# Optimization experiments

Hardware: AMD Instinct MI355X
Metric: run time of the kernel (lower is better)

Reference implementation:

```python
import jax, jax.numpy as jnp
import numpy as np
from jax import lax

B, T, D, H = 4, 4096, 1024, 8
DK, DV = 1024, 2048          # expand_k=1.0, expand_v=2.0
RANK, MAXL, LOOPD = 16, 8, 128  # lora_rank, max_loops, dim*loop_dim_fraction
THRESH = 0.99
EPS = 1e-6
GK_SCALE = 16.0              # GLA forget-gate temperature


def setup_inputs() -> dict:
    key = jax.random.key(0)
    ks = jax.random.split(key, 16)
    r = lambda i, shape, s=0.02: jax.random.normal(ks[i], shape, jnp.float32) * s
    return {
        "h": jax.random.normal(ks[0], (B, T, D), jnp.float32),
        "e": jax.random.normal(ks[1], (B, T, D), jnp.float32),
        "norm_w": jnp.ones((D,), jnp.float32),
        "out_norm_w": jnp.ones((D,), jnp.float32),
        "Wq": r(2, (D, DK)), "Wk": r(3, (D, DK)), "Wv": r(4, (D, DV)),
        "Wgk": r(5, (D, DK)), "Wg": r(6, (D, DV)), "Wo": r(7, (DV, D)),
        "lora_A": r(8, (MAXL, D, RANK)), "lora_B": r(9, (MAXL, RANK, D)),
        "inj_A": 0.9 * jnp.eye(D, dtype=jnp.float32) + r(10, (D, D)),
        "inj_B": r(11, (D, D)),
        "act_w": r(12, (D,)),
        "act_b": jnp.full((), -2.0, jnp.float32),  # gradual halting
        "loop_table": r(13, (MAXL, LOOPD)),
        "n_loops": 4,
    }


def rmsnorm(x, w):
    return x * lax.rsqrt(jnp.mean(x * x, axis=-1, keepdims=True) + EPS) * w


def gla(x, Wq, Wk, Wv, Wgk, Wg, Wo, num_heads):
    """Gated Linear Attention: data-dependent forget gates, linear-time recurrent scan."""
    b, t, d = x.shape
    dk, dv = Wq.shape[1], Wv.shape[1]
    dkh, dvh = dk // num_heads, dv // num_heads
    q = (x @ Wq).reshape(b, t, num_heads, dkh) * (dkh ** -0.5)
    k = (x @ Wk).reshape(b, t, num_heads, dkh)
    v = (x @ Wv).reshape(b, t, num_heads, dvh)
    # forget gate alpha in (0,1): exp(logsigmoid(gk)/16)
    alpha = jnp.exp(jax.nn.log_sigmoid(x @ Wgk) / GK_SCALE).reshape(b, t, num_heads, dkh)

    def step(S, qkva):  # S: (b, H, dkh, dvh)
        qt, kt, vt, at = qkva
        S = at[..., None] * S + kt[..., None] * vt[..., None, :]
        ot = jnp.einsum('bhk,bhkv->bhv', qt, S)
        return S, ot

    S0 = jnp.zeros((b, num_heads, dkh, dvh), x.dtype)
    xs = (jnp.swapaxes(q, 0, 1), jnp.swapaxes(k, 0, 1),
          jnp.swapaxes(v, 0, 1), jnp.swapaxes(alpha, 0, 1))
    _, o = lax.scan(step, S0, xs)                  # o: (t, b, H, dvh)
    o = jnp.swapaxes(o, 0, 1).reshape(b, t, dv)
    o = o * jax.nn.silu(x @ Wg)                    # output gate
    return o @ Wo


def reference(h, e, norm_w, out_norm_w, Wq, Wk, Wv, Wgk, Wg, Wo,
              lora_A, lora_B, inj_A, inj_B, act_w, act_b, loop_table, n_loops):
    b, t_len, d = h.shape
    halted = jnp.zeros((b, t_len), bool)
    cum = jnp.zeros((b, t_len), h.dtype)
    h_out = jnp.zeros_like(h)
    loopd = loop_table.shape[1]
    for t in range(n_loops):  # small fixed depth loop (structurally distinct LoRA/embed per t)
        # loop index embedding on first loopd channels
        h = h.at[..., :loopd].add(loop_table[t])
        h_norm = rmsnorm(h + e, norm_w)
        g = gla(h_norm, Wq, Wk, Wv, Wgk, Wg, Wo, H)   # dropout: eval mode (identity)
        g = g + (g @ lora_A[t]) @ lora_B[t]            # depth LoRA
        h = h @ inj_A.T + e @ inj_B.T + g              # LTI injection: A.h + B.e + gla
        # ACT halting accumulate
        p = jax.nn.sigmoid(h @ act_w + act_b)          # (b, t_len)
        running = ~halted
        p_eff = jnp.where(running, p, jnp.zeros_like(p))
        new_cum = cum + p_eff
        newly = running & (new_cum >= THRESH)
        w = jnp.where(newly, 1.0 - cum, p_eff)         # remainder for newly-halted
        h_out = h_out + w[..., None] * h
        cum = new_cum
        halted = halted | newly
    return rmsnorm(h_out, out_norm_w)
```

## Files before the change

### kernel.cpp

```cpp
#include <hip/hip_runtime.h>

#define BB 4
#define TT 4096
#define DD 1024
#define HH 8
#define DKK 1024
#define DVV 2048
#define MR (BB*TT)
#define DKH 128
#define DVH 256
#define NLOOPS 4
#define LCH 128
#define NCH (TT/LCH)
#define PADW 136
#define NPROJ 7168

#define WS_NEED 662310912ull

__device__ __attribute__((aligned(256))) unsigned char g_ws[WS_NEED];

typedef __bf16 bf16x8 __attribute__((ext_vector_type(8)));
typedef float  f32x4  __attribute__((ext_vector_type(4)));

union GemmSmem {
    unsigned short ab[2][128 * 32];
    unsigned short c16[128 * 136];
    float cf[64 * 140];
};

__device__ __forceinline__ unsigned short f2bfu(float f) {
    unsigned int u = __builtin_bit_cast(unsigned int, f);
    u += 0x7fffu + ((u >> 16) & 1u);
    return (unsigned short)(u >> 16);
}
__device__ __forceinline__ float bfu2f(unsigned short s) {
    unsigned int u = ((unsigned int)s) << 16;
    return __builtin_bit_cast(float, u);
}

__device__ __forceinline__ void gld_lds16(const void* g, void* l) {
    __builtin_amdgcn_global_load_lds(
        (__attribute__((address_space(1))) void*)const_cast<void*>(g),
        (__attribute__((address_space(3))) void*)l, 16, 0, 0);
}

__global__ __launch_bounds__(256) void k_transpose_bf16(
    const float* __restrict__ in, unsigned short* __restrict__ out, int K, int N)
{
    __shared__ float tile[64][65];
    int k0 = blockIdx.y * 64, n0 = blockIdx.x * 64;
    int tx = threadIdx.x & 63, ty = threadIdx.x >> 6;
    #pragma unroll
    for (int r = 0; r < 64; r += 4)
        tile[ty + r][tx] = in[(size_t)(k0 + ty + r) * N + n0 + tx];
    __syncthreads();
    #pragma unroll
    for (int r = 0; r < 64; r += 4)
        out[(size_t)(n0 + ty + r) * K + k0 + tx] = f2bfu(tile[tx][ty + r]);
}

__global__ __launch_bounds__(256) void k_conv_e(
    const float* __restrict__ e, unsigned short* __restrict__ he)
{
    size_t gid = (size_t)blockIdx.x * 256 + threadIdx.x;
    size_t b4 = gid * 4;
    size_t row = b4 >> 10; int col = (int)(b4 & 1023);
    float4 v = *(const float4*)&e[row * 1024 + col];
    *(ushort4*)&he[row * 2048 + 1024 + col] =
        make_ushort4(f2bfu(v.x), f2bfu(v.y), f2bfu(v.z), f2bfu(v.w));
}

__global__ __launch_bounds__(256) void k_conv_injcomb(
    const float* __restrict__ injA, const float* __restrict__ injB,
    unsigned short* __restrict__ WinjT, float* __restrict__ diag)
{
    int idx = blockIdx.x * 256 + threadIdx.x;
    int i = idx >> 10, j = idx & 1023;
    float va = injA[idx], vb = injB[idx];
    unsigned short ua;
    if (i == j) { diag[i] = va; ua = 0; }
    else        { ua = f2bfu(va); }
    WinjT[(size_t)i * 2048 + j] = ua;
    WinjT[(size_t)i * 2048 + 1024 + j] = f2bfu(vb);
}

__global__ __launch_bounds__(256) void k_prep(
    float* __restrict__ h, const float* __restrict__ e,
    const float* __restrict__ norm_w, const float* __restrict__ ltab,
    unsigned short* __restrict__ he, unsigned short* __restrict__ xn_bf)
{
    int row = blockIdx.x, tid = threadIdx.x;
    size_t base = (size_t)row * DD + tid * 4;
    float4 hv = *(float4*)&h[base];
    if (tid < 32) {
        float4 lv = *(const float4*)&ltab[tid * 4];
        hv.x += lv.x; hv.y += lv.y; hv.z += lv.z; hv.w += lv.w;
        *(float4*)&h[base] = hv;
    }
    float4 ev = *(const float4*)&e[base];
    float sx = hv.x + ev.x, sy = hv.y + ev.y, sz = hv.z + ev.z, sw = hv.w + ev.w;
    float partial = sx*sx + sy*sy + sz*sz + sw*sw;
    __shared__ float red[256];
    red[tid] = partial; __syncthreads();
    for (int st = 128; st > 0; st >>= 1) {
        if (tid < st) red[tid] += red[tid + st];
        __syncthreads();
    }
    float rms = rsqrtf(red[0] * (1.0f / DD) + 1e-6f);
    float4 wv = *(const float4*)&norm_w[tid * 4];
    *(ushort4*)&xn_bf[base] = make_ushort4(
        f2bfu(sx * rms * wv.x), f2bfu(sy * rms * wv.y),
        f2bfu(sz * rms * wv.z), f2bfu(sw * rms * wv.w));
    *(ushort4*)&he[(size_t)row * 2048 + tid * 4] =
        make_ushort4(f2bfu(hv.x), f2bfu(hv.y), f2bfu(hv.z), f2bfu(hv.w));
}

__global__ __launch_bounds__(256) void k_gemm_proj(
    const unsigned short* __restrict__ A, const unsigned short* __restrict__ Bt,
    unsigned short* __restrict__ qout, unsigned short* __restrict__ kout,
    float* __restrict__ lgout, unsigned short* __restrict__ vout,
    unsigned short* __restrict__ xgout, float qscale)
{
    __shared__ GemmSmem sm;
    unsigned short* lsA = sm.ab[0];
    unsigned short* lsB = sm.ab[1];
    int tid = threadIdx.x, lane = tid & 63, wave = tid >> 6;
    int wm = wave >> 1, wn = wave & 1;
    int bm = blockIdx.y * 128, bn = blockIdx.x * 128;
    int lrow = lane >> 2, lcol = (lane & 3) * 8;
    const int K = 1024;

    f32x4 acc[4][4];
    #pragma unroll
    for (int i = 0; i < 4; ++i)
        #pragma unroll
        for (int j = 0; j < 4; ++j) { f32x4 z = {0,0,0,0}; acc[i][j] = z; }

    for (int k0 = 0; k0 < K; k0 += 32) {
        __syncthreads();
        #pragma unroll
        for (int r = 0; r < 2; ++r) {
            int row = r * 64 + wave * 16 + lrow;
            gld_lds16(A  + (size_t)(bm + row) * K + k0 + lcol, &lsA[row * 32 + lcol]);
            gld_lds16(Bt + (size_t)(bn + row) * K + k0 + lcol, &lsB[row * 32 + lcol]);
        }
        __syncthreads();
        int quad = lane >> 4, mr = lane & 15;
        bf16x8 av[4], bv[4];
        #pragma unroll
        for (int t2 = 0; t2 < 4; ++t2) {
            av[t2] = *(const bf16x8*)&lsA[(wm * 64 + t2 * 16 + mr) * 32 + quad * 8];
            bv[t2] = *(const bf16x8*)&lsB[(wn * 64 + t2 * 16 + mr) * 32 + quad * 8];
        }
        #pragma unroll
        for (int tm = 0; tm < 4; ++tm)
            #pragma unroll
            for (int tn = 0; tn < 4; ++tn)
                acc[tm][tn] = __builtin_amdgcn_mfma_f32_16x16x32_bf16(
                    av[tm], bv[tn], acc[tm][tn], 0, 0, 0);
    }

    int quad = lane >> 4, mr = lane & 15;
    __syncthreads();

    if (bn >= 2048 && bn < 3072) {
        int cb = bn - 2048;
        #pragma unroll 1
        for (int half = 0; half < 2; ++half) {
            if (wm == half) {
                #pragma unroll
                for (int tm = 0; tm < 4; ++tm)
                    #pragma unroll
                    for (int tn = 0; tn < 4; ++tn)
                        #pragma unroll
                        for (int r = 0; r < 4; ++r) {
                            float v = acc[tm][tn][r];
                            v = (fminf(v, 0.f) - log1pf(expf(-fabsf(v)))) * 0.0625f;
                            sm.cf[(tm * 16 + quad * 4 + r) * 140 + wn * 64 + tn * 16 + mr] = v;
                        }
            }
            __syncthreads();
            #pragma unroll
            for (int ps = 0; ps < 8; ++ps) {
                int idx = ps * 256 + tid;
                int rl = idx >> 5, c4 = (idx & 31) * 4;
                float4 vv = *(float4*)&sm.cf[rl * 140 + c4];
                *(float4*)&lgout[(size_t)(bm + half * 64 + rl) * 1024 + cb + c4] = vv;
            }
            __syncthreads();
        }
    } else {
        unsigned short* obuf; int stride, cb;
        float scale = 1.f;
        if (bn < 1024)      { obuf = qout;  stride = 1024; cb = bn;        scale = qscale; }
        else if (bn < 2048) { obuf = kout;  stride = 1024; cb = bn - 1024; }
        else if (bn < 5120) { obuf = vout;  stride = 2048; cb = bn - 3072; }
        else                { obuf = xgout; stride = 2048; cb = bn - 5120; }
        #pragma unroll
        for (int tm = 0; tm < 4; ++tm)
            #pragma unroll
            for (int tn = 0; tn < 4; ++tn)
                #pragma unroll
                for (int r = 0; r < 4; ++r)
                    sm.c16[(wm * 64 + tm * 16 + quad * 4 + r) * 136
                           + wn * 64 + tn * 16 + mr] = f2bfu(acc[tm][tn][r] * scale);
        __syncthreads();
        #pragma unroll
        for (int ps = 0; ps < 8; ++ps) {
            int idx = ps * 256 + tid;
            int rl = idx >> 4, c8 = (idx & 15) * 8;
            int4 w = *(int4*)&sm.c16[rl * 136 + c8];
            *(int4*)&obuf[(size_t)(bm + rl) * stride + cb + c8] = w;
        }
    }
}

template<int HASADD, int HASDIAG>
__global__ __launch_bounds__(256) void k_gemm_f32(
    const unsigned short* __restrict__ A, const unsigned short* __restrict__ Bt,
    float* __restrict__ out, const float* __restrict__ addend,
    const float* __restrict__ hsrc, const float* __restrict__ diag,
    int N, int K)
{
    __shared__ GemmSmem sm;
    unsigned short* lsA = sm.ab[0];
    unsigned short* lsB = sm.ab[1];
    int tid = threadIdx.x, lane = tid & 63, wave = tid >> 6;
    int wm = wave >> 1, wn = wave & 1;
    int bm = blockIdx.y * 128, bn = blockIdx.x * 128;
    int lrow = lane >> 2, lcol = (lane & 3) * 8;

    f32x4 acc[4][4];
    #pragma unroll
    for (int i = 0; i < 4; ++i)
        #pragma unroll
        for (int j = 0; j < 4; ++j) { f32x4 z = {0,0,0,0}; acc[i][j] = z; }

    for (int k0 = 0; k0 < K; k0 += 32) {
        __syncthreads();
        #pragma unroll
        for (int r = 0; r < 2; ++r) {
            int row = r * 64 + wave * 16 + lrow;
            gld_lds16(A  + (size_t)(bm + row) * K + k0 + lcol, &lsA[row * 32 + lcol]);
            gld_lds16(Bt + (size_t)(bn + row) * K + k0 + lcol, &lsB[row * 32 + lcol]);
        }
        __syncthreads();
        int quad = lane >> 4, mr = lane & 15;
        bf16x8 av[4], bv[4];
        #pragma unroll
        for (int t2 = 0; t2 < 4; ++t2) {
            av[t2] = *(const bf16x8*)&lsA[(wm * 64 + t2 * 16 + mr) * 32 + quad * 8];
            bv[t2] = *(const bf16x8*)&lsB[(wn * 64 + t2 * 16 + mr) * 32 + quad * 8];
        }
        #pragma unroll
        for (int tm = 0; tm < 4; ++tm)
            #pragma unroll
            for (int tn = 0; tn < 4; ++tn)
                acc[tm][tn] = __builtin_amdgcn_mfma_f32_16x16x32_bf16(
                    av[tm], bv[tn], acc[tm][tn], 0, 0, 0);
    }

    int quad = lane >> 4, mr = lane & 15;
    __syncthreads();
    #pragma unroll 1
    for (int half = 0; half < 2; ++half) {
        if (wm == half) {
            #pragma unroll
            for (int tm = 0; tm < 4; ++tm)
                #pragma unroll
                for (int tn = 0; tn < 4; ++tn)
                    #pragma unroll
                    for (int r = 0; r < 4; ++r)
                        sm.cf[(tm * 16 + quad * 4 + r) * 140
                              + wn * 64 + tn * 16 + mr] = acc[tm][tn][r];
        }
        __syncthreads();
        #pragma unroll
        for (int ps = 0; ps < 8; ++ps) {
            int idx = ps * 256 + tid;
            int rl = idx >> 5, c4 = (idx & 31) * 4;
            float4 vv = *(float4*)&sm.cf[rl * 140 + c4];
            size_t oi = (size_t)(bm + half * 64 + rl) * N + bn + c4;
            if (HASDIAG) {
                float4 hh = *(const float4*)&hsrc[oi];
                float4 dd = *(const float4*)&diag[bn + c4];
                vv.x += hh.x * dd.x; vv.y += hh.y * dd.y;
                vv.z += hh.z * dd.z; vv.w += hh.w * dd.w;
            }
            if (HASADD) {
                float4 aa = *(const float4*)&addend[oi];
                vv.x += aa.x; vv.y += aa.y; vv.z += aa.z; vv.w += aa.w;
            }
            *(float4*)&out[oi] = vv;
        }
        __syncthreads();
    }
}

__global__ __launch_bounds__(128) void k_c1(
    const float* __restrict__ lg, unsigned short* __restrict__ q,
    unsigned short* __restrict__ kk, float* __restrict__ dLe)
{
    int chunk = blockIdx.x, bh = blockIdx.y;
    int b = bh >> 3, h = bh & 7;
    int i = threadIdx.x;
    size_t r0 = (size_t)b * TT + (size_t)chunk * LCH;
    float c = 0.f, e = 1.f;
    for (int t = 0; t < LCH; ++t) {
        size_t off = (r0 + t) * DKK + h * DKH + i;
        c += lg[off];
        e = __expf(c);
        float ei = __expf(-c);
        q[off] = f2bfu(bfu2f(q[off]) * e);
        kk[off] = f2bfu(bfu2f(kk[off]) * ei);
    }
    dLe[((size_t)chunk * 32 + bh) * DKH + i] = e;
}

__global__ __launch_bounds__(256, 1) void k_c2(
    const unsigned short* __restrict__ q, const unsigned short* __restrict__ kk,
    const unsigned short* __restrict__ v, unsigned short* __restrict__ ob,
    float* __restrict__ U)
{
    extern __shared__ unsigned short smd[];
    unsigned short* lQ  = smd;
    unsigned short* lK  = smd + LCH * PADW;
    unsigned short* lKT = smd + 2 * LCH * PADW;
    unsigned short* lVT = smd + 3 * LCH * PADW;

    int chunk = blockIdx.x, bh = blockIdx.y;
    int b = bh >> 3, h = bh & 7;
    int tid = threadIdx.x, lane = tid & 63, wave = tid >> 6;
    int wm = wave >> 1, wn = wave & 1;
    int quad = lane >> 4, mr = lane & 15;
    size_t r0 = (size_t)b * TT + (size_t)chunk * LCH;

    #pragma unroll
    for (int ps = 0; ps < 8; ++ps) {
        int idx = ps * 256 + tid;
        int row = idx >> 4, c8 = (idx & 15) * 8;
        size_t g = (r0 + row) * DKK + h * DKH + c8;
        *(int4*)&lQ[row * PADW + c8] = *(const int4*)&q[g];
        union { int4 w; unsigned short u[8]; } tmp;
        tmp.w = *(const int4*)&kk[g];
        *(int4*)&lK[row * PADW + c8] = tmp.w;
        #pragma unroll
        for (int u2 = 0; u2 < 8; ++u2)
            lKT[(c8 + u2) * PADW + row] = tmp.u[u2];
    }
    __syncthreads();

    f32x4 pa[4][4];
    #pragma unroll
    for (int i = 0; i < 4; ++i)
        #pragma unroll
        for (int j = 0; j < 4; ++j) { f32x4 z = {0,0,0,0}; pa[i][j] = z; }
    for (int k0 = 0; k0 < DKH; k0 += 32) {
        bf16x8 av[4], bv[4];
        #pragma unroll
        for (int t2 = 0; t2 < 4; ++t2) {
            av[t2] = *(const bf16x8*)&lQ[(wm * 64 + t2 * 16 + mr) * PADW + k0 + quad * 8];
            bv[t2] = *(const bf16x8*)&lK[(wn * 64 + t2 * 16 + mr) * PADW + k0 + quad * 8];
        }
        #pragma unroll
        for (int tm = 0; tm < 4; ++tm)
            #pragma unroll
            for (int tn = 0; tn < 4; ++tn)
                pa[tm][tn] = __builtin_amdgcn_mfma_f32_16x16x32_bf16(
                    av[tm], bv[tn], pa[tm][tn], 0, 0, 0);
    }
    __syncthreads();

    #pragma unroll
    for (int tm = 0; tm < 4; ++tm)
        #pragma unroll
        for (int tn = 0; tn < 4; ++tn)
            #pragma unroll
            for (int r = 0; r < 4; ++r) {
                int trow = wm * 64 + tm * 16 + quad * 4 + r;
                int scol = wn * 64 + tn * 16 + mr;
                float pv = (trow >= scol) ? pa[tm][tn][r] : 0.f;
                lQ[trow * PADW + scol] = f2bfu(pv);
            }
    #pragma unroll
    for (int ps = 0; ps < 8; ++ps) {
        int idx = ps * 256 + tid;
        int s = idx >> 4, j8 = (idx & 15) * 8;
        size_t g = (r0 + s) * DVV + h * DVH + j8;
        union { int4 w; unsigned short u[8]; } tmp;
        tmp.w = *(const int4*)&v[g];
        #pragma unroll
        for (int u2 = 0; u2 < 8; ++u2)
            lVT[(j8 + u2) * PADW + s] = tmp.u[u2];
    }
    __syncthreads();

    #pragma unroll 1
    for (int panel = 0; panel < 2; ++panel) {
        f32x4 oa[4][4], ua[4][4];
        #pragma unroll
        for (int i = 0; i < 4; ++i)
            #pragma unroll
            for (int j = 0; j < 4; ++j) { f32x4 z = {0,0,0,0}; oa[i][j] = z; ua[i][j] = z; }
        for (int k0 = 0; k0 < LCH; k0 += 32) {
            bf16x8 pv[4], kt[4], vb[4];
            #pragma unroll
            for (int t2 = 0; t2 < 4; ++t2) {
                pv[t2] = *(const bf16x8*)&lQ [(wm * 64 + t2 * 16 + mr) * PADW + k0 + quad * 8];
                kt[t2] = *(const bf16x8*)&lKT[(wm * 64 + t2 * 16 + mr) * PADW + k0 + quad * 8];
                vb[t2] = *(const bf16x8*)&lVT[(wn * 64 + t2 * 16 + mr) * PADW + k0 + quad * 8];
            }
            #pragma unroll
            for (int tm = 0; tm < 4; ++tm)
                #pragma unroll
                for (int tn = 0; tn < 4; ++tn) {
                    oa[tm][tn] = __builtin_amdgcn_mfma_f32_16x16x32_bf16(
                        pv[tm], vb[tn], oa[tm][tn], 0, 0, 0);
                    ua[tm][tn] = __builtin_amdgcn_mfma_f32_16x16x32_bf16(
                        kt[tm], vb[tn], ua[tm][tn], 0, 0, 0);
                }
        }
        #pragma unroll
        for (int tm = 0; tm < 4; ++tm)
            #pragma unroll
            for (int tn = 0; tn < 4; ++tn)
                #pragma unroll
                for (int r = 0; r < 4; ++r) {
                    int m_ = wm * 64 + tm * 16 + quad * 4 + r;
                    int j_ = panel * 128 + wn * 64 + tn * 16 + mr;
                    ob[(r0 + m_) * DVV + h * DVH + j_] = f2bfu(oa[tm][tn][r]);
                    U[(((size_t)chunk * 32 + bh) * DKH + m_) * DVH + j_] = ua[tm][tn][r];
                }
        __syncthreads();
        if (panel == 0) {
            #pragma unroll
            for (int ps = 0; ps < 8; ++ps) {
                int idx = ps * 256 + tid;
                int s = idx >> 4, j8 = (idx & 15) * 8;
                size_t g = (r0 + s) * DVV + h * DVH + 128 + j8;
                union { int4 w; unsigned short u[8]; } tmp;
                tmp.w = *(const int4*)&v[g];
                #pragma unroll
                for (int u2 = 0; u2 < 8; ++u2)
                    lVT[(j8 + u2) * PADW + s] = tmp.u[u2];
            }
            __syncthreads();
        }
    }
}

__global__ __launch_bounds__(256) void k_c3(
    float* __restrict__ U, const float* __restrict__ dLe)
{
    int gid = blockIdx.x * 256 + threadIdx.x;
    int bh = gid >> 13;
    int rem = gid & 8191;
    int i = rem >> 6, j4 = rem & 63;
    float4 S = make_float4(0.f, 0.f, 0.f, 0.f);
    for (int c = 0; c < NCH; ++c) {
        size_t off = (((size_t)c * 32 + bh) * DKH + i) * DVH + j4 * 4;
        float4 u = *(float4*)&U[off];
        *(float4*)&U[off] = S;
        float d = dLe[((size_t)c * 32 + bh) * DKH + i];
        S.x = d * (S.x + u.x); S.y = d * (S.y + u.y);
        S.z = d * (S.z + u.z); S.w = d * (S.w + u.w);
    }
}

__global__ __launch_bounds__(256, 1) void k_c4(
    const unsigned short* __restrict__ q, const float* __restrict__ S,
    unsigned short* __restrict__ ob, const unsigned short* __restrict__ xg)
{
    extern __shared__ unsigned short smd[];
    unsigned short* lQ  = smd;
    unsigned short* lST = smd + LCH * PADW;

    int chunk = blockIdx.x, bh = blockIdx.y;
    int b = bh >> 3, h = bh & 7;
    int tid = threadIdx.x, lane = tid & 63, wave = tid >> 6;
    int wm = wave >> 1, wn = wave & 1;
    int quad = lane >> 4, mr = lane & 15;
    size_t r0 = (size_t)b * TT + (size_t)chunk * LCH;

    #pragma unroll
    for (int ps = 0; ps < 8; ++ps) {
        int idx = ps * 256 + tid;
        int row = idx >> 4, c8 = (idx & 15) * 8;
        size_t g = (r0 + row) * DKK + h * DKH + c8;
        *(int4*)&lQ[row * PADW + c8] = *(const int4*)&q[g];
    }

    #pragma unroll 1
    for (int panel = 0; panel < 2; ++panel) {
        __syncthreads();
        #pragma unroll
        for (int ps = 0; ps < 16; ++ps) {
            int idx = ps * 256 + tid;
            int i = idx >> 5, j4 = idx & 31;
            float4 sv = *(const float4*)&S[(((size_t)chunk * 32 + bh) * DKH + i) * DVH
                                           + panel * 128 + j4 * 4];
            lST[(j4 * 4 + 0) * PADW + i] = f2bfu(sv.x);
            lST[(j4 * 4 + 1) * PADW + i] = f2bfu(sv.y);
            lST[(j4 * 4 + 2) * PADW + i] = f2bfu(sv.z);
            lST[(j4 * 4 + 3) * PADW + i] = f2bfu(sv.w);
        }
        __syncthreads();

        f32x4 oa[4][4];
        #pragma unroll
        for (int i = 0; i < 4; ++i)
            #pragma unroll
            for (int j = 0; j < 4; ++j) { f32x4 z = {0,0,0,0}; oa[i][j] = z; }
        for (int k0 = 0; k0 < DKH; k0 += 32) {
            bf16x8 av[4], bv[4];
            #pragma unroll
            for (int t2 = 0; t2 < 4; ++t2) {
                av[t2] = *(const bf16x8*)&lQ [(wm * 64 + t2 * 16 + mr) * PADW + k0 + quad * 8];
                bv[t2] = *(const bf16x8*)&lST[(wn * 64 + t2 * 16 + mr) * PADW + k0 + quad * 8];
            }
            #pragma unroll
            for (int tm = 0; tm < 4; ++tm)
                #pragma unroll
                for (int tn = 0; tn < 4; ++tn)
                    oa[tm][tn] = __builtin_amdgcn_mfma_f32_16x16x32_bf16(
                        av[tm], bv[tn], oa[tm][tn], 0, 0, 0);
        }
        #pragma unroll
        for (int tm = 0; tm < 4; ++tm)
            #pragma unroll
            for (int tn = 0; tn < 4; ++tn)
                #pragma unroll
                for (int r = 0; r < 4; ++r) {
                    int t_ = wm * 64 + tm * 16 + quad * 4 + r;
                    int j_ = panel * 128 + wn * 64 + tn * 16 + mr;
                    size_t oi = (r0 + t_) * DVV + h * DVH + j_;
                    float ov = bfu2f(ob[oi]) + oa[tm][tn][r];
                    float xf = bfu2f(xg[oi]);
                    ob[oi] = f2bfu(ov * xf / (1.f + expf(-xf)));
                }
    }
}

__global__ __launch_bounds__(256) void k_lora1(
    const float* __restrict__ G, const float* __restrict__ A, float* __restrict__ tmp)
{
    int row = blockIdx.x * 4 + (threadIdx.x >> 6);
    int lane = threadIdx.x & 63;
    float acc[16];
    #pragma unroll
    for (int r = 0; r < 16; ++r) acc[r] = 0.f;
    const float* grow = G + (size_t)row * DD;
    for (int k2 = lane; k2 < DD; k2 += 64) {
        float g = grow[k2];
        const float4* ar = (const float4*)(A + k2 * 16);
        float4 a0 = ar[0], a1 = ar[1], a2 = ar[2], a3 = ar[3];
        acc[0] = fmaf(g, a0.x, acc[0]);  acc[1] = fmaf(g, a0.y, acc[1]);
        acc[2] = fmaf(g, a0.z, acc[2]);  acc[3] = fmaf(g, a0.w, acc[3]);
        acc[4] = fmaf(g, a1.x, acc[4]);  acc[5] = fmaf(g, a1.y, acc[5]);
        acc[6] = fmaf(g, a1.z, acc[6]);  acc[7] = fmaf(g, a1.w, acc[7]);
        acc[8] = fmaf(g, a2.x, acc[8]);  acc[9] = fmaf(g, a2.y, acc[9]);
        acc[10] = fmaf(g, a2.z, acc[10]); acc[11] = fmaf(g, a2.w, acc[11]);
        acc[12] = fmaf(g, a3.x, acc[12]); acc[13] = fmaf(g, a3.y, acc[13]);
        acc[14] = fmaf(g, a3.z, acc[14]); acc[15] = fmaf(g, a3.w, acc[15]);
    }
    #pragma unroll
    for (int off = 32; off >= 1; off >>= 1)
        #pragma unroll
        for (int r = 0; r < 16; ++r) acc[r] += __shfl_xor(acc[r], off);
    if (lane == 0) {
        #pragma unroll
        for (int r = 0; r < 16; ++r) tmp[(size_t)row * 16 + r] = acc[r];
    }
}

__global__ __launch_bounds__(256) void k_lora2(
    float* __restrict__ G, const float* __restrict__ tmp, const float* __restrict__ Bm)
{
    int row = blockIdx.x, tid = threadIdx.x;
    __shared__ float t16[16];
    if (tid < 16) t16[tid] = tmp[(size_t)row * 16 + tid];
    __syncthreads();
    size_t base = (size_t)row * DD + tid * 4;
    float4 acc = *(float4*)&G[base];
    #pragma unroll
    for (int r = 0; r < 16; ++r) {
        float tv = t16[r];
        float4 bv = *(const float4*)&Bm[r * DD + tid * 4];
        acc.x = fmaf(tv, bv.x, acc.x); acc.y = fmaf(tv, bv.y, acc.y);
        acc.z = fmaf(tv, bv.z, acc.z); acc.w = fmaf(tv, bv.w, acc.w);
    }
    *(float4*)&G[base] = acc;
}

__global__ __launch_bounds__(256) void k_act(
    const float* __restrict__ h, const float* __restrict__ act_w,
    const float* __restrict__ act_b, float* __restrict__ out,
    float* __restrict__ cum, int* __restrict__ halted)
{
    int row = blockIdx.x, tid = threadIdx.x;
    size_t base = (size_t)row * DD + tid * 4;
    float4 hv = *(const float4*)&h[base];
    float4 wv = *(const float4*)&act_w[tid * 4];
    float partial = hv.x*wv.x + hv.y*wv.y + hv.z*wv.z + hv.w*wv.w;
    __shared__ float red[256];
    __shared__ float s_cm;
    __shared__ int s_hl;
    if (tid == 0) { s_cm = cum[row]; s_hl = halted[row]; }
    red[tid] = partial; __syncthreads();
    for (int st = 128; st > 0; st >>= 1) {
        if (tid < st) red[tid] += red[tid + st];
        __syncthreads();
    }
    float p = 1.f / (1.f + expf(-(red[0] + act_b[0])));
    float cm = s_cm;
    int hl = s_hl;
    float p_eff = hl ? 0.f : p;
    float ncum = cm + p_eff;
    int newly = (!hl) && (ncum >= 0.99f);
    float w = newly ? (1.f - cm) : p_eff;
    float4 ho = *(float4*)&out[base];
    ho.x += w * hv.x; ho.y += w * hv.y; ho.z += w * hv.z; ho.w += w * hv.w;
    *(float4*)&out[base] = ho;
    if (tid == 0) { cum[row] = ncum; halted[row] = hl | newly; }
}

__global__ __launch_bounds__(256) void k_final(
    float* __restrict__ io, const float* __restrict__ w)
{
    int row = blockIdx.x, tid = threadIdx.x;
    size_t base = (size_t)row * DD + tid * 4;
    float4 hv = *(const float4*)&io[base];
    float partial = hv.x*hv.x + hv.y*hv.y + hv.z*hv.z + hv.w*hv.w;
    __shared__ float red[256];
    red[tid] = partial; __syncthreads();
    for (int st = 128; st > 0; st >>= 1) {
        if (tid < st) red[tid] += red[tid + st];
        __syncthreads();
    }
    float rms = rsqrtf(red[0] * (1.0f / DD) + 1e-6f);
    float4 wv = *(const float4*)&w[tid * 4];
    float4 o = make_float4(hv.x*rms*wv.x, hv.y*rms*wv.y, hv.z*rms*wv.z, hv.w*rms*wv.w);
    *(float4*)&io[base] = o;
}

extern "C" void kernel_launch(void* const* d_in, const int* in_sizes, int n_in,
                              void* d_out, int out_size, void* d_ws, size_t ws_size,
                              hipStream_t stream)
{
    const float* in_h       = (const float*)d_in[0];
    const float* in_e       = (const float*)d_in[1];
    const float* norm_w     = (const float*)d_in[2];
    const float* out_norm_w = (const float*)d_in[3];
    const float* Wq   = (const float*)d_in[4];
    const float* Wk   = (const float*)d_in[5];
    const float* Wv   = (const float*)d_in[6];
    const float* Wgk  = (const float*)d_in[7];
    const float* Wg   = (const float*)d_in[8];
    const float* Wo   = (const float*)d_in[9];
    const float* lora_A = (const float*)d_in[10];
    const float* lora_B = (const float*)d_in[11];
    const float* inj_A  = (const float*)d_in[12];
    const float* inj_B  = (const float*)d_in[13];
    const float* act_w  = (const float*)d_in[14];
    const float* act_b  = (const float*)d_in[15];
    const float* loop_table = (const float*)d_in[16];

    char* p;
    if (ws_size >= WS_NEED) {
        p = (char*)d_ws;
    } else {
        void* sym = nullptr;
        hipGetSymbolAddress(&sym, HIP_SYMBOL(g_ws));
        p = (char*)sym;
    }

    float* h      = (float*)p;            p += (size_t)MR * DD * 4;
    unsigned short* he_bf = (unsigned short*)p; p += (size_t)MR * 2048 * 2;
    unsigned short* xn_bf = (unsigned short*)p; p += (size_t)MR * DD * 2;
    unsigned short* q_bf  = (unsigned short*)p; p += (size_t)MR * DKK * 2;
    unsigned short* k_bf  = (unsigned short*)p; p += (size_t)MR * DKK * 2;
    unsigned short* v_bf  = (unsigned short*)p; p += (size_t)MR * DVV * 2;
    unsigned short* xg_bf = (unsigned short*)p; p += (size_t)MR * DVV * 2;
    float* lgbuf  = (float*)p;            p += (size_t)MR * DKK * 4;
    unsigned short* ob0   = (unsigned short*)p; p += (size_t)MR * DVV * 2;
    float* U      = (float*)p;            p += (size_t)NCH * 32 * DKH * DVH * 4;
    float* dLe    = (float*)p;            p += (size_t)NCH * 32 * DKH * 4;
    unsigned short* WprojT = (unsigned short*)p; p += (size_t)NPROJ * DKK * 2;
    unsigned short* WoT    = (unsigned short*)p; p += (size_t)DD * DVV * 2;
    unsigned short* WinjT  = (unsigned short*)p; p += (size_t)DD * 2048 * 2;
    float* diagA = (float*)p;             p += DD * 4;
    float* tmp16 = (float*)p;             p += (size_t)MR * 16 * 4;
    float* cum   = (float*)p;             p += MR * 4;
    int*   halted = (int*)p;              p += MR * 4;
    float* g2 = lgbuf;
    float* h_out = (float*)d_out;

    hipMemcpyAsync(h, in_h, (size_t)MR * DD * 4, hipMemcpyDeviceToDevice, stream);
    hipMemsetAsync(h_out, 0, (size_t)MR * DD * 4, stream);
    hipMemsetAsync(cum, 0, MR * 4, stream);
    hipMemsetAsync(halted, 0, MR * 4, stream);

    k_transpose_bf16<<<dim3(16, 16), 256, 0, stream>>>(Wq,  WprojT,              DD, DKK);
    k_transpose_bf16<<<dim3(16, 16), 256, 0, stream>>>(Wk,  WprojT + 1024*1024,  DD, DKK);
    k_transpose_bf16<<<dim3(16, 16), 256, 0, stream>>>(Wgk, WprojT + 2048*1024,  DD, DKK);
    k_transpose_bf16<<<dim3(32, 16), 256, 0, stream>>>(Wv,  WprojT + 3072*1024,  DD, DVV);
    k_transpose_bf16<<<dim3(32, 16), 256, 0, stream>>>(Wg,  WprojT + (size_t)5120*1024, DD, DVV);
    k_transpose_bf16<<<dim3(16, 32), 256, 0, stream>>>(Wo,  WoT, DVV, DD);
    k_conv_injcomb<<<4096, 256, 0, stream>>>(inj_A, inj_B, WinjT, diagA);
    k_conv_e<<<MR * DD / 1024, 256, 0, stream>>>(in_e, he_bf);

    const float qscale = 0.08838834764831845f;

    for (int t = 0; t < NLOOPS; ++t) {
        k_prep<<<MR, 256, 0, stream>>>(h, in_e, norm_w, loop_table + t * 128, he_bf, xn_bf);

        k_gemm_proj<<<dim3(NPROJ/128, MR/128), 256, 0, stream>>>(
            xn_bf, WprojT, q_bf, k_bf, lgbuf, v_bf, xg_bf, qscale);

        k_c1<<<dim3(NCH, 32), 128, 0, stream>>>(lgbuf, q_bf, k_bf, dLe);
        k_c2<<<dim3(NCH, 32), 256, 4 * LCH * PADW * 2, stream>>>(
            q_bf, k_bf, v_bf, ob0, U);
        k_c3<<<1024, 256, 0, stream>>>(U, dLe);
        k_c4<<<dim3(NCH, 32), 256, 2 * LCH * PADW * 2, stream>>>(q_bf, U, ob0, xg_bf);

        k_gemm_f32<0,0><<<dim3(DD/128, MR/128), 256, 0, stream>>>(
            ob0, WoT, g2, nullptr, nullptr, nullptr, DD, DVV);

        k_lora1<<<MR / 4, 256, 0, stream>>>(g2, lora_A + (size_t)t * DD * 16, tmp16);
        k_lora2<<<MR, 256, 0, stream>>>(g2, tmp16, lora_B + (size_t)t * 16 * DD);

        k_gemm_f32<1,1><<<dim3(DD/128, MR/128), 256, 0, stream>>>(
            he_bf, WinjT, h, g2, h, diagA, DD, 2048);

        k_act<<<MR, 256, 0, stream>>>(h, act_w, act_b, h_out, cum, halted);
    }

    k_final<<<MR, 256, 0, stream>>>(h_out, out_norm_w);
}
```

Before: 4.818 ms.

## Replace GEMMs with 256x256 8-wave double-buffered swizzled LDS kernels

Measured after the change: 4.257 ms. 11.7% less time.

```diff
diff --git a/kernel.cpp b/kernel.cpp
--- a/kernel.cpp
+++ b/kernel.cpp
@@ -22,12 +22,6 @@
 typedef __bf16 bf16x8 __attribute__((ext_vector_type(8)));
 typedef float  f32x4  __attribute__((ext_vector_type(4)));
 
-union GemmSmem {
-    unsigned short ab[2][128 * 32];
-    unsigned short c16[128 * 136];
-    float cf[64 * 140];
-};
-
 __device__ __forceinline__ unsigned short f2bfu(float f) {
     unsigned int u = __builtin_bit_cast(unsigned int, f);
     u += 0x7fffu + ((u >> 16) & 1u);
@@ -115,79 +109,139 @@
         make_ushort4(f2bfu(hv.x), f2bfu(hv.y), f2bfu(hv.z), f2bfu(hv.w));
 }
 
-__global__ __launch_bounds__(256) void k_gemm_proj(
+template<int KB>
+__device__ __forceinline__ void gemm8_core(
+    const char* __restrict__ Ab, const char* __restrict__ Bb,
+    int bm, int bn, char* sm, f32x4 (&acc)[8][4])
+{
+    constexpr int NKT = KB / 128;
+    const int tid = threadIdx.x;
+    const int lane = tid & 63;
+    const int wave = tid >> 6;
+    const int wm = wave >> 2, wn = wave & 3;
+    const int ln15 = lane & 15, q4 = lane >> 4;
+    const int xorv = (ln15 & 7) << 4;
+    const int xc0 = (q4 * 16) ^ xorv;
+    const int xc1 = (64 + q4 * 16) ^ xorv;
+
+    const int L0 = tid * 16;
+    const int L1 = 8192 + tid * 16;
+    const int lin0 = L0 ^ (((L0 >> 7) & 7) << 4);
+    const int lin1 = L1 ^ (((L1 >> 7) & 7) << 4);
+    const int sr0 = lin0 >> 7, sc0 = lin0 & 127;
+    const int sr1 = lin1 >> 7, sc1 = lin1 & 127;
+
+    auto STAGE = [&](const char* gb, int row0, int kcol, int region) {
+        gld_lds16(gb + (size_t)(row0 + sr0) * KB + (kcol + sc0), sm + region + L0);
+        gld_lds16(gb + (size_t)(row0 + sr1) * KB + (kcol + sc1), sm + region + L1);
+    };
+    auto STAGE_R = [&](int r, int bufo, int kcol) {
+        if (r == 0)      STAGE(Ab, bm,       kcol, bufo);
+        else if (r == 1) STAGE(Bb, bn,       kcol, bufo + 32768);
+        else if (r == 2) STAGE(Bb, bn + 128, kcol, bufo + 49152);
+        else             STAGE(Ab, bm + 128, kcol, bufo + 16384);
+    };
+    auto QUAD = [&](int r, int bufo) {
+        const int mh = r >> 1, nh = r & 1;
+        const char* As = sm + bufo;
+        const char* Bs = sm + bufo + 32768;
+        bf16x8 av[4][2], bv[2][2];
+        #pragma unroll
+        for (int i2 = 0; i2 < 4; ++i2) {
+            const char* rp = As + (mh * 128 + wm * 64 + i2 * 16 + ln15) * 128;
+            av[i2][0] = *(const bf16x8*)(rp + xc0);
+            av[i2][1] = *(const bf16x8*)(rp + xc1);
+        }
+        #pragma unroll
+        for (int j2 = 0; j2 < 2; ++j2) {
+            const char* rp = Bs + (nh * 128 + wn * 32 + j2 * 16 + ln15) * 128;
+            bv[j2][0] = *(const bf16x8*)(rp + xc0);
+            bv[j2][1] = *(const bf16x8*)(rp + xc1);
+        }
+        __builtin_amdgcn_s_setprio(1);
+        #pragma unroll
+        for (int i2 = 0; i2 < 4; ++i2)
+            #pragma unroll
+            for (int j2 = 0; j2 < 2; ++j2) {
+                acc[mh*4+i2][nh*2+j2] = __builtin_amdgcn_mfma_f32_16x16x32_bf16(
+                    av[i2][0], bv[j2][0], acc[mh*4+i2][nh*2+j2], 0, 0, 0);
+                acc[mh*4+i2][nh*2+j2] = __builtin_amdgcn_mfma_f32_16x16x32_bf16(
+                    av[i2][1], bv[j2][1], acc[mh*4+i2][nh*2+j2], 0, 0, 0);
+            }
+        __builtin_amdgcn_s_setprio(0);
+    };
+
+    STAGE_R(0, 0, 0); STAGE_R(1, 0, 0); STAGE_R(2, 0, 0); STAGE_R(3, 0, 0);
+
+    #pragma unroll 2
+    for (int kt = 0; kt < NKT - 1; ++kt) {
+        const int cbufo = (kt & 1) << 16;
+        const int sbufo = cbufo ^ 65536;
+        const int kcol = (kt + 1) * 128;
+        #pragma unroll
+        for (int r = 0; r < 4; ++r) {
+            STAGE_R(r, sbufo, kcol);
+            asm volatile("s_waitcnt vmcnt(6)" ::: "memory");
+            asm volatile("s_barrier" ::: "memory");
+            QUAD(r, cbufo);
+        }
+        asm volatile("s_barrier" ::: "memory");
+    }
+    {
+        const int cbufo = ((NKT - 1) & 1) << 16;
+        asm volatile("s_waitcnt vmcnt(4)" ::: "memory");
+        asm volatile("s_barrier" ::: "memory");
+        QUAD(0, cbufo);
+        asm volatile("s_waitcnt vmcnt(2)" ::: "memory");
+        asm volatile("s_barrier" ::: "memory");
+        QUAD(1, cbufo);
+        asm volatile("s_waitcnt vmcnt(0)" ::: "memory");
+        asm volatile("s_barrier" ::: "memory");
+        QUAD(2, cbufo);
+        QUAD(3, cbufo);
+    }
+}
+
+__global__ __launch_bounds__(512, 2) void k_gemm_proj8(
     const unsigned short* __restrict__ A, const unsigned short* __restrict__ Bt,
     unsigned short* __restrict__ qout, unsigned short* __restrict__ kout,
     float* __restrict__ lgout, unsigned short* __restrict__ vout,
     unsigned short* __restrict__ xgout, float qscale)
 {
-    __shared__ GemmSmem sm;
-    unsigned short* lsA = sm.ab[0];
-    unsigned short* lsB = sm.ab[1];
-    int tid = threadIdx.x, lane = tid & 63, wave = tid >> 6;
-    int wm = wave >> 1, wn = wave & 1;
-    int bm = blockIdx.y * 128, bn = blockIdx.x * 128;
-    int lrow = lane >> 2, lcol = (lane & 3) * 8;
-    const int K = 1024;
-
-    f32x4 acc[4][4];
-    #pragma unroll
-    for (int i = 0; i < 4; ++i)
+    extern __shared__ char sm[];
+    int bid = blockIdx.x;
+    int nb = (bid & 7) * 224 + (bid >> 3);
+    int bm = (nb / 28) * 256, bn = (nb % 28) * 256;
+
+    f32x4 acc[8][4];
+    #pragma unroll
+    for (int i = 0; i < 8; ++i)
         #pragma unroll
         for (int j = 0; j < 4; ++j) { f32x4 z = {0,0,0,0}; acc[i][j] = z; }
 
-    for (int k0 = 0; k0 < K; k0 += 32) {
-        __syncthreads();
-        #pragma unroll
-        for (int r = 0; r < 2; ++r) {
-            int row = r * 64 + wave * 16 + lrow;
-            gld_lds16(A  + (size_t)(bm + row) * K + k0 + lcol, &lsA[row * 32 + lcol]);
-            gld_lds16(Bt + (size_t)(bn + row) * K + k0 + lcol, &lsB[row * 32 + lcol]);
-        }
-        __syncthreads();
-        int quad = lane >> 4, mr = lane & 15;
-        bf16x8 av[4], bv[4];
-        #pragma unroll
-        for (int t2 = 0; t2 < 4; ++t2) {
-            av[t2] = *(const bf16x8*)&lsA[(wm * 64 + t2 * 16 + mr) * 32 + quad * 8];
-            bv[t2] = *(const bf16x8*)&lsB[(wn * 64 + t2 * 16 + mr) * 32 + quad * 8];
-        }
-        #pragma unroll
-        for (int tm = 0; tm < 4; ++tm)
-            #pragma unroll
-            for (int tn = 0; tn < 4; ++tn)
-                acc[tm][tn] = __builtin_amdgcn_mfma_f32_16x16x32_bf16(
-                    av[tm], bv[tn], acc[tm][tn], 0, 0, 0);
-    }
-
-    int quad = lane >> 4, mr = lane & 15;
-    __syncthreads();
+    gemm8_core<2048>((const char*)A, (const char*)Bt, bm, bn, sm, acc);
+
+    const int tid = threadIdx.x, lane = tid & 63, wave = tid >> 6;
+    const int wm = wave >> 2, wn = wave & 3;
+    const int ln15 = lane & 15, q4 = lane >> 4;
 
     if (bn >= 2048 && bn < 3072) {
         int cb = bn - 2048;
-        #pragma unroll 1
-        for (int half = 0; half < 2; ++half) {
-            if (wm == half) {
+        #pragma unroll
+        for (int fm = 0; fm < 8; ++fm) {
+            int mh = fm >> 2, i2 = fm & 3;
+            int rowb = bm + mh * 128 + wm * 64 + i2 * 16 + q4 * 4;
+            #pragma unroll
+            for (int fn = 0; fn < 4; ++fn) {
+                int nh = fn >> 1, j2 = fn & 1;
+                int col = cb + nh * 128 + wn * 32 + j2 * 16 + ln15;
                 #pragma unroll
-                for (int tm = 0; tm < 4; ++tm)
-                    #pragma unroll
-                    for (int tn = 0; tn < 4; ++tn)
-                        #pragma unroll
-                        for (int r = 0; r < 4; ++r) {
-                            float v = acc[tm][tn][r];
-                            v = (fminf(v, 0.f) - log1pf(expf(-fabsf(v)))) * 0.0625f;
-                            sm.cf[(tm * 16 + quad * 4 + r) * 140 + wn * 64 + tn * 16 + mr] = v;
-                        }
+                for (int r = 0; r < 4; ++r) {
+                    float v = acc[fm][fn][r];
+                    v = (fminf(v, 0.f) - log1pf(expf(-fabsf(v)))) * 0.0625f;
+                    lgout[(size_t)(rowb + r) * 1024 + col] = v;
+                }
             }
-            __syncthreads();
-            #pragma unroll
-            for (int ps = 0; ps < 8; ++ps) {
-                int idx = ps * 256 + tid;
-                int rl = idx >> 5, c4 = (idx & 31) * 4;
-                float4 vv = *(float4*)&sm.cf[rl * 140 + c4];
-                *(float4*)&lgout[(size_t)(bm + half * 64 + rl) * 1024 + cb + c4] = vv;
-            }
-            __syncthreads();
         }
     } else {
         unsigned short* obuf; int stride, cb;
@@ -197,103 +251,66 @@
         else if (bn < 5120) { obuf = vout;  stride = 2048; cb = bn - 3072; }
         else                { obuf = xgout; stride = 2048; cb = bn - 5120; }
         #pragma unroll
-        for (int tm = 0; tm < 4; ++tm)
-            #pragma unroll
-            for (int tn = 0; tn < 4; ++tn)
+        for (int fm = 0; fm < 8; ++fm) {
+            int mh = fm >> 2, i2 = fm & 3;
+            int rowb = bm + mh * 128 + wm * 64 + i2 * 16 + q4 * 4;
+            #pragma unroll
+            for (int fn = 0; fn < 4; ++fn) {
+                int nh = fn >> 1, j2 = fn & 1;
+                int col = cb + nh * 128 + wn * 32 + j2 * 16 + ln15;
                 #pragma unroll
                 for (int r = 0; r < 4; ++r)
-                    sm.c16[(wm * 64 + tm * 16 + quad * 4 + r) * 136
-                           + wn * 64 + tn * 16 + mr] = f2bfu(acc[tm][tn][r] * scale);
-        __syncthreads();
-        #pragma unroll
-        for (int ps = 0; ps < 8; ++ps) {
-            int idx = ps * 256 + tid;
-            int rl = idx >> 4, c8 = (idx & 15) * 8;
-            int4 w = *(int4*)&sm.c16[rl * 136 + c8];
-            *(int4*)&obuf[(size_t)(bm + rl) * stride + cb + c8] = w;
-        }
-    }
-}
-
-template<int HASADD, int HASDIAG>
-__global__ __launch_bounds__(256) void k_gemm_f32(
+                    obuf[(size_t)(rowb + r) * stride + col] =
+                        f2bfu(acc[fm][fn][r] * scale);
+            }
+        }
+    }
+}
+
+template<int HASADD, int HASDIAG, int KB>
+__global__ __launch_bounds__(512, 2) void k_gemm8_f32(
     const unsigned short* __restrict__ A, const unsigned short* __restrict__ Bt,
     float* __restrict__ out, const float* __restrict__ addend,
-    const float* __restrict__ hsrc, const float* __restrict__ diag,
-    int N, int K)
-{
-    __shared__ GemmSmem sm;
-    unsigned short* lsA = sm.ab[0];
-    unsigned short* lsB = sm.ab[1];
-    int tid = threadIdx.x, lane = tid & 63, wave = tid >> 6;
-    int wm = wave >> 1, wn = wave & 1;
-    int bm = blockIdx.y * 128, bn = blockIdx.x * 128;
-    int lrow = lane >> 2, lcol = (lane & 3) * 8;
-
-    f32x4 acc[4][4];
-    #pragma unroll
-    for (int i = 0; i < 4; ++i)
+    const float* __restrict__ hsrc, const float* __restrict__ diag, int N)
+{
+    extern __shared__ char sm[];
+    int bid = blockIdx.x;
+    int cpx = gridDim.x >> 3;
+    int nb = (bid & 7) * cpx + (bid >> 3);
+    int nbn = N >> 8;
+    int bm = (nb / nbn) * 256, bn = (nb % nbn) * 256;
+
+    f32x4 acc[8][4];
+    #pragma unroll
+    for (int i = 0; i < 8; ++i)
         #pragma unroll
         for (int j = 0; j < 4; ++j) { f32x4 z = {0,0,0,0}; acc[i][j] = z; }
 
-    for (int k0 = 0; k0 < K; k0 += 32) {
-        __syncthreads();
-        #pragma unroll
-        for (int r = 0; r < 2; ++r) {
-            int row = r * 64 + wave * 16 + lrow;
-            gld_lds16(A  + (size_t)(bm + row) * K + k0 + lcol, &lsA[row * 32 + lcol]);
-            gld_lds16(Bt + (size_t)(bn + row) * K + k0 + lcol, &lsB[row * 32 + lcol]);
-        }
-        __syncthreads();
-        int quad = lane >> 4, mr = lane & 15;
-        bf16x8 av[4], bv[4];
-        #pragma unroll
-        for (int t2 = 0; t2 < 4; ++t2) {
-            av[t2] = *(const bf16x8*)&lsA[(wm * 64 + t2 * 16 + mr) * 32 + quad * 8];
-            bv[t2] = *(const bf16x8*)&lsB[(wn * 64 + t2 * 16 + mr) * 32 + quad * 8];
-        }
-        #pragma unroll
-        for (int tm = 0; tm < 4; ++tm)
-            #pragma unroll
-            for (int tn = 0; tn < 4; ++tn)
-                acc[tm][tn] = __builtin_amdgcn_mfma_f32_16x16x32_bf16(
-                    av[tm], bv[tn], acc[tm][tn], 0, 0, 0);
-    }
-
-    int quad = lane >> 4, mr = lane & 15;
-    __syncthreads();
-    #pragma unroll 1
-    for (int half = 0; half < 2; ++half) {
-        if (wm == half) {
-            #pragma unroll
-            for (int tm = 0; tm < 4; ++tm)
-                #pragma unroll
-                for (int tn = 0; tn < 4; ++tn)
-                    #pragma unroll
-                    for (int r = 0; r < 4; ++r)
-                        sm.cf[(tm * 16 + quad * 4 + r) * 140
-                              + wn * 64 + tn * 16 + mr] = acc[tm][tn][r];
-        }
-        __syncthreads();
-        #pragma unroll
-        for (int ps = 0; ps < 8; ++ps) {
-            int idx = ps * 256 + tid;
-            int rl = idx >> 5, c4 = (idx & 31) * 4;
-            float4 vv = *(float4*)&sm.cf[rl * 140 + c4];
-            size_t oi = (size_t)(bm + half * 64 + rl) * N + bn + c4;
-            if (HASDIAG) {
-                float4 hh = *(const float4*)&hsrc[oi];
-                float4 dd = *(const float4*)&diag[bn + c4];
-                vv.x += hh.x * dd.x; vv.y += hh.y * dd.y;
-                vv.z += hh.z * dd.z; vv.w += hh.w * dd.w;
+    gemm8_core<KB>((const char*)A, (const char*)Bt, bm, bn, sm, acc);
+
+    const int tid = threadIdx.x, lane = tid & 63, wave = tid >> 6;
+    const int wm = wave >> 2, wn = wave & 3;
+    const int ln15 = lane & 15, q4 = lane >> 4;
+
+    #pragma unroll
+    for (int fm = 0; fm < 8; ++fm) {
+        int mh = fm >> 2, i2 = fm & 3;
+        int rowb = bm + mh * 128 + wm * 64 + i2 * 16 + q4 * 4;
+        #pragma unroll
+        for (int fn = 0; fn < 4; ++fn) {
+            int nh = fn >> 1, j2 = fn & 1;
+            int col = bn + nh * 128 + wn * 32 + j2 * 16 + ln15;
+            float dg = 0.f;
+            if (HASDIAG) dg = diag[col];
+            #pragma unroll
+            for (int r = 0; r < 4; ++r) {
+                size_t oi = (size_t)(rowb + r) * N + col;
+                float v = acc[fm][fn][r];
+                if (HASDIAG) v += hsrc[oi] * dg;
+                if (HASADD)  v += addend[oi];
+                out[oi] = v;
             }
-            if (HASADD) {
-                float4 aa = *(const float4*)&addend[oi];
-                vv.x += aa.x; vv.y += aa.y; vv.z += aa.z; vv.w += aa.w;
-            }
-            *(float4*)&out[oi] = vv;
-        }
-        __syncthreads();
+        }
     }
 }
 
@@ -714,7 +731,7 @@
     for (int t = 0; t < NLOOPS; ++t) {
         k_prep<<<MR, 256, 0, stream>>>(h, in_e, norm_w, loop_table + t * 128, he_bf, xn_bf);
 
-        k_gemm_proj<<<dim3(NPROJ/128, MR/128), 256, 0, stream>>>(
+        k_gemm_proj8<<<1792, 512, 131072, stream>>>(
             xn_bf, WprojT, q_bf, k_bf, lgbuf, v_bf, xg_bf, qscale);
 
         k_c1<<<dim3(NCH, 32), 128, 0, stream>>>(lgbuf, q_bf, k_bf, dLe);
@@ -723,14 +740,14 @@
         k_c3<<<1024, 256, 0, stream>>>(U, dLe);
         k_c4<<<dim3(NCH, 32), 256, 2 * LCH * PADW * 2, stream>>>(q_bf, U, ob0, xg_bf);
 
-        k_gemm_f32<0,0><<<dim3(DD/128, MR/128), 256, 0, stream>>>(
-            ob0, WoT, g2, nullptr, nullptr, nullptr, DD, DVV);
+        k_gemm8_f32<0, 0, 4096><<<256, 512, 131072, stream>>>(
+            ob0, WoT, g2, nullptr, nullptr, nullptr, DD);
 
         k_lora1<<<MR / 4, 256, 0, stream>>>(g2, lora_A + (size_t)t * DD * 16, tmp16);
         k_lora2<<<MR, 256, 0, stream>>>(g2, tmp16, lora_B + (size_t)t * 16 * DD);
 
-        k_gemm_f32<1,1><<<dim3(DD/128, MR/128), 256, 0, stream>>>(
-            he_bf, WinjT, h, g2, h, diagA, DD, 2048);
+        k_gemm8_f32<1, 1, 4096><<<256, 512, 131072, stream>>>(
+            he_bf, WinjT, h, g2, h, diagA, DD);
 
         k_act<<<MR, 256, 0, stream>>>(h, act_w, act_b, h_out, cum, halted);
     }
```
